# Optimization experiments

Hardware: AMD Instinct MI355X
Metric: run time of the kernel (lower is better)

## Reference

```python
import jax, jax.numpy as jnp
import numpy as np

N_HEAD = 16
N_EMBD = 1024
B, T = 4, 2048


def setup_inputs() -> dict:
    key = jax.random.key(0)
    ks = jax.random.split(key, 5)
    s_in = 1.0 / np.sqrt(N_EMBD)
    return {
        "x": jax.random.normal(ks[0], (B, T, N_EMBD), dtype=jnp.float32),
        "W_qkv": jax.random.normal(ks[1], (N_EMBD, 3 * N_EMBD), dtype=jnp.float32) * s_in,
        "b_qkv": jnp.zeros((3 * N_EMBD,), dtype=jnp.float32),
        "W_proj": jax.random.normal(ks[2], (N_EMBD, N_EMBD), dtype=jnp.float32) * s_in,
        "b_proj": jnp.zeros((N_EMBD,), dtype=jnp.float32),
    }


def reference(x, W_qkv, b_qkv, W_proj, b_proj):
    Bb, Tt, C = x.shape
    H = N_HEAD
    hd = C // H  # head dim
    qkv = x @ W_qkv + b_qkv                      # [B,T,3C]
    q, k, v = jnp.split(qkv, 3, axis=-1)
    # [B,H,T,hd]
    q = q.reshape(Bb, Tt, H, hd).transpose(0, 2, 1, 3)
    k = k.reshape(Bb, Tt, H, hd).transpose(0, 2, 1, 3)
    v = v.reshape(Bb, Tt, H, hd).transpose(0, 2, 1, 3)
    scale = 1.0 / np.sqrt(hd).astype(np.float32)
    att = jnp.einsum("bhqd,bhkd->bhqk", q, k) * scale
    causal = jnp.tril(jnp.ones((Tt, Tt), dtype=bool))
    att = jnp.where(causal, att, jnp.float32(-jnp.inf))
    att = jax.nn.softmax(att, axis=-1)
    y = jnp.einsum("bhqk,bhkd->bhqd", att, v)    # [B,H,T,hd]
    y = y.transpose(0, 2, 1, 3).reshape(Bb, Tt, C)
    return y @ W_proj + b_proj
```

## Files before the change

### kernel.cpp

```cpp
#include <hip/hip_runtime.h>
#include <hip/hip_bf16.h>
#include <math.h>

typedef unsigned short u16;
typedef __bf16 bf16_t;
typedef bf16_t bf16x8 __attribute__((ext_vector_type(8)));
typedef float f32x4 __attribute__((ext_vector_type(4)));

#define N_HEADC 16
#define C_EMBD  1024
#define B_SZ    4
#define T_SEQ   2048
#define HD      64
#define M_TOT   (B_SZ * T_SEQ)

__device__ __forceinline__ float b2f(u16 x) {
    return __uint_as_float(((unsigned)x) << 16);
}
__device__ __forceinline__ u16 f2b(float f) {
    unsigned u = __float_as_uint(f);
    u = u + 0x7fffu + ((u >> 16) & 1u);
    return (u16)(u >> 16);
}
__device__ __forceinline__ unsigned pack2f(float a, float b) {
    unsigned ua = (__float_as_uint(a) + 0x8000u) >> 16;
    unsigned ub = (__float_as_uint(b) + 0x8000u) & 0xffff0000u;
    return ua | ub;
}
__device__ __forceinline__ float fexp2(float x) {
#if __has_builtin(__builtin_amdgcn_exp2f)
    return __builtin_amdgcn_exp2f(x);
#else
    return exp2f(x);
#endif
}
__device__ __forceinline__ void gl_lds16(const u16* g, u16* l) {
    __builtin_amdgcn_global_load_lds(
        (const __attribute__((address_space(1))) unsigned int*)g,
        (__attribute__((address_space(3))) unsigned int*)l,
        16, 0, 0);
}


__global__ __launch_bounds__(256) void cast_f32_to_bf16(const float* __restrict__ in,
                                                        u16* __restrict__ out) {
    int i = (blockIdx.x * 256 + threadIdx.x) * 4;
    float4 v = *(const float4*)(in + i);
    ushort4 o;
    o.x = f2b(v.x); o.y = f2b(v.y); o.z = f2b(v.z); o.w = f2b(v.w);
    *(ushort4*)(out + i) = o;
}

__global__ __launch_bounds__(256) void transpose_cast(const float* __restrict__ in,
                                                      u16* __restrict__ out,
                                                      int K, int N) {
    __shared__ float tile[32][33];
    int n0 = blockIdx.x * 32, k0 = blockIdx.y * 32;
    for (int i = threadIdx.y; i < 32; i += 8)
        tile[i][threadIdx.x] = in[(size_t)(k0 + i) * N + n0 + threadIdx.x];
    __syncthreads();
    for (int i = threadIdx.y; i < 32; i += 8)
        out[(size_t)(n0 + i) * K + k0 + threadIdx.x] = f2b(tile[threadIdx.x][i]);
}

__global__ __launch_bounds__(256) void gemm_qkv(const u16* __restrict__ A,
                                                const u16* __restrict__ BT,
                                                const float* __restrict__ bias,
                                                u16* __restrict__ qQ,
                                                u16* __restrict__ qK,
                                                u16* __restrict__ qVt) {
    const int K = C_EMBD;
    __shared__ __align__(16) u16 sA[128 * 32];
    __shared__ __align__(16) u16 sB[128 * 32];
    int m0 = blockIdx.y * 128;
    int n0 = blockIdx.x * 128;
    int tid = threadIdx.x;
    int w = tid >> 6, lane = tid & 63;
    int m_off = (w & 1) * 64, n_off = (w >> 1) * 64;
    int quad = lane >> 4, rl = lane & 15;

    f32x4 acc[4][4];
    #pragma unroll
    for (int i = 0; i < 4; ++i)
        #pragma unroll
        for (int j = 0; j < 4; ++j)
            acc[i][j] = f32x4{0.f, 0.f, 0.f, 0.f};

    int srow = lane >> 2, sko = (lane & 3) * 8;

    for (int k0 = 0; k0 < K; k0 += 32) {
        #pragma unroll
        for (int c = 0; c < 4; ++c) {
            int rb = ((w & 1) * 4 + c) * 16;
            if (w < 2)
                gl_lds16(&A[(size_t)(m0 + rb + srow) * K + k0 + sko], &sA[rb * 32]);
            else
                gl_lds16(&BT[(size_t)(n0 + rb + srow) * K + k0 + sko], &sB[rb * 32]);
        }
        __syncthreads();
        bf16x8 af[4], bfr[4];
        #pragma unroll
        for (int i = 0; i < 4; ++i)
            af[i] = *(const bf16x8*)&sA[(m_off + i * 16 + rl) * 32 + quad * 8];
        #pragma unroll
        for (int j = 0; j < 4; ++j)
            bfr[j] = *(const bf16x8*)&sB[(n_off + j * 16 + rl) * 32 + quad * 8];
        #pragma unroll
        for (int i = 0; i < 4; ++i)
            #pragma unroll
            for (int j = 0; j < 4; ++j)
                acc[i][j] = __builtin_amdgcn_mfma_f32_16x16x32_bf16(af[i], bfr[j], acc[i][j], 0, 0, 0);
        __syncthreads();
    }

    const float QSC = 0.18033688011112042f;
    #pragma unroll
    for (int j = 0; j < 4; ++j) {
        int n = n0 + n_off + j * 16 + rl;
        float bv = bias[n];
        int p = n >> 10, cch = n & 1023;
        int h = cch >> 6, d = cch & 63;
        #pragma unroll
        for (int i = 0; i < 4; ++i) {
            int mbase = m0 + m_off + i * 16 + quad * 4;
            int bb = mbase >> 11, t0 = mbase & 2047;
            size_t thbase = ((size_t)bb * N_HEADC + h) * T_SEQ;
            if (p == 0) {
                #pragma unroll
                for (int r = 0; r < 4; ++r)
                    qQ[(thbase + t0 + r) * HD + d] = f2b((acc[i][j][r] + bv) * QSC);
            } else if (p == 1) {
                #pragma unroll
                for (int r = 0; r < 4; ++r)
                    qK[(thbase + t0 + r) * HD + d] = f2b(acc[i][j][r] + bv);
            } else {
                ushort4 o;
                o.x = f2b(acc[i][j][0] + bv);
                o.y = f2b(acc[i][j][1] + bv);
                o.z = f2b(acc[i][j][2] + bv);
                o.w = f2b(acc[i][j][3] + bv);
                *(ushort4*)&qVt[(((size_t)bb * N_HEADC + h) * HD + d) * T_SEQ + t0] = o;
            }
        }
    }
}

__global__ __launch_bounds__(256) void gemm_proj(const u16* __restrict__ A,
                                                 const u16* __restrict__ BT,
                                                 const float* __restrict__ bias,
                                                 float* __restrict__ out) {
    const int K = C_EMBD;
    __shared__ __align__(16) u16 sA[128 * 32];
    __shared__ __align__(16) u16 sB[128 * 32];
    int m0 = blockIdx.y * 128;
    int n0 = blockIdx.x * 128;
    int tid = threadIdx.x;
    int w = tid >> 6, lane = tid & 63;
    int m_off = (w & 1) * 64, n_off = (w >> 1) * 64;
    int quad = lane >> 4, rl = lane & 15;

    f32x4 acc[4][4];
    #pragma unroll
    for (int i = 0; i < 4; ++i)
        #pragma unroll
        for (int j = 0; j < 4; ++j)
            acc[i][j] = f32x4{0.f, 0.f, 0.f, 0.f};

    int srow = lane >> 2, sko = (lane & 3) * 8;

    for (int k0 = 0; k0 < K; k0 += 32) {
        #pragma unroll
        for (int c = 0; c < 4; ++c) {
            int rb = ((w & 1) * 4 + c) * 16;
            if (w < 2)
                gl_lds16(&A[(size_t)(m0 + rb + srow) * K + k0 + sko], &sA[rb * 32]);
            else
                gl_lds16(&BT[(size_t)(n0 + rb + srow) * K + k0 + sko], &sB[rb * 32]);
        }
        __syncthreads();
        bf16x8 af[4], bfr[4];
        #pragma unroll
        for (int i = 0; i < 4; ++i)
            af[i] = *(const bf16x8*)&sA[(m_off + i * 16 + rl) * 32 + quad * 8];
        #pragma unroll
        for (int j = 0; j < 4; ++j)
            bfr[j] = *(const bf16x8*)&sB[(n_off + j * 16 + rl) * 32 + quad * 8];
        #pragma unroll
        for (int i = 0; i < 4; ++i)
            #pragma unroll
            for (int j = 0; j < 4; ++j)
                acc[i][j] = __builtin_amdgcn_mfma_f32_16x16x32_bf16(af[i], bfr[j], acc[i][j], 0, 0, 0);
        __syncthreads();
    }

    #pragma unroll
    for (int i = 0; i < 4; ++i) {
        int mbase = m0 + m_off + i * 16 + quad * 4;
        #pragma unroll
        for (int j = 0; j < 4; ++j) {
            int n = n0 + n_off + j * 16 + rl;
            float bv = bias[n];
            #pragma unroll
            for (int r = 0; r < 4; ++r)
                out[(size_t)(mbase + r) * C_EMBD + n] = acc[i][j][r] + bv;
        }
    }
}

__global__ __launch_bounds__(256) void attn_mfma(const u16* __restrict__ Qg,
                                                 const u16* __restrict__ Kg,
                                                 const u16* __restrict__ Vtg,
                                                 u16* __restrict__ yb) {
    int bx = blockIdx.x, h = blockIdx.y, b = blockIdx.z;
    const size_t hs = (size_t)T_SEQ * HD;
    const u16* Qp  = Qg  + ((size_t)b * N_HEADC + h) * hs;
    const u16* Kp  = Kg  + ((size_t)b * N_HEADC + h) * hs;
    const u16* Vtp = Vtg + ((size_t)b * N_HEADC + h) * hs;

    __shared__ __align__(16) u16 sK[2][2][64][32];
    __shared__ __align__(16) u16 sVt[2][2][64][32];
    __shared__ __align__(16) u16 sP[4][32][72];

    int tid = threadIdx.x;
    int lane = tid & 63, w = tid >> 6;
    int quad = lane >> 4, rl = lane & 15;
    u16* sPw = &sP[w][0][0];
    int srow = lane >> 2;
    int sch = (lane & 3) * 8;
    const f32x4 zf = {0.f, 0.f, 0.f, 0.f};
    const float SOFT_M = 16.0f;

    #pragma unroll
    for (int phase = 0; phase < 2; ++phase) {
        int qt = phase == 0 ? (15 - bx) : bx;
        int q0w = qt * 128 + w * 32;
        int nkt = 2 * qt + 2;

        bf16x8 qf[2][2];
        #pragma unroll
        for (int nt = 0; nt < 2; ++nt)
            #pragma unroll
            for (int ks = 0; ks < 2; ++ks)
                qf[nt][ks] = *(const bf16x8*)&Qp[(size_t)(q0w + nt * 16 + rl) * HD + ks * 32 + quad * 8];

        f32x4 O[2][4];
        #pragma unroll
        for (int mi = 0; mi < 2; ++mi)
            #pragma unroll
            for (int nd = 0; nd < 4; ++nd)
                O[mi][nd] = f32x4{0.f, 0.f, 0.f, 0.f};
        float l_[2] = {0.f, 0.f};

        __syncthreads();
        #pragma unroll
        for (int c = 0; c < 4; ++c) {
            int lc = w * 4 + c;
            int ks = (lc >> 2) & 1;
            int rb = (lc & 3) * 16;
            if (lc < 8)
                gl_lds16(Kp + (size_t)(rb + srow) * HD + ks * 32 + sch, &sK[0][ks][rb][0]);
            else
                gl_lds16(Vtp + (size_t)(rb + srow) * T_SEQ + ks * 32 + sch, &sVt[0][ks][rb][0]);
        }

        for (int kt = 0; kt < nkt; ++kt) {
            __syncthreads();
            int buf = kt & 1;
            int k0 = kt * 64;
            if (kt + 1 < nkt) {
                int k1 = k0 + 64;
                #pragma unroll
                for (int c = 0; c < 4; ++c) {
                    int lc = w * 4 + c;
                    int ks = (lc >> 2) & 1;
                    int rb = (lc & 3) * 16;
                    if (lc < 8)
                        gl_lds16(Kp + (size_t)(k1 + rb + srow) * HD + ks * 32 + sch,
                                 &sK[buf ^ 1][ks][rb][0]);
                    else
                        gl_lds16(Vtp + (size_t)(rb + srow) * T_SEQ + k1 + ks * 32 + sch,
                                 &sVt[buf ^ 1][ks][rb][0]);
                }
            }
            if (k0 > q0w + 31) continue;

            f32x4 st[4][2];
            #pragma unroll
            for (int mt = 0; mt < 4; ++mt) {
                bf16x8 ak0 = *(const bf16x8*)&sK[buf][0][mt * 16 + rl][quad * 8];
                bf16x8 ak1 = *(const bf16x8*)&sK[buf][1][mt * 16 + rl][quad * 8];
                #pragma unroll
                for (int nt = 0; nt < 2; ++nt) {
                    f32x4 t = __builtin_amdgcn_mfma_f32_16x16x32_bf16(ak0, qf[nt][0], zf, 0, 0, 0);
                    st[mt][nt] = __builtin_amdgcn_mfma_f32_16x16x32_bf16(ak1, qf[nt][1], t, 0, 0, 0);
                }
            }

            if (k0 + 63 > q0w) {
                #pragma unroll
                for (int mt = 0; mt < 4; ++mt)
                    #pragma unroll
                    for (int nt = 0; nt < 2; ++nt)
                        #pragma unroll
                        for (int r = 0; r < 4; ++r) {
                            int kpos = k0 + mt * 16 + quad * 4 + r;
                            int q = q0w + nt * 16 + rl;
                            if (kpos > q) st[mt][nt][r] = -INFINITY;
                        }
            }

            #pragma unroll
            for (int nt = 0; nt < 2; ++nt) {
                float lsum = 0.f;
                #pragma unroll
                for (int mt = 0; mt < 4; ++mt) {
                    float p0 = fexp2(st[mt][nt][0] - SOFT_M);
                    float p1 = fexp2(st[mt][nt][1] - SOFT_M);
                    float p2 = fexp2(st[mt][nt][2] - SOFT_M);
                    float p3 = fexp2(st[mt][nt][3] - SOFT_M);
                    lsum += (p0 + p1) + (p2 + p3);
                    *(uint2*)&sPw[(nt * 16 + rl) * 72 + mt * 16 + quad * 4] =
                        make_uint2(pack2f(p0, p1), pack2f(p2, p3));
                }
                l_[nt] += lsum;
            }

            #pragma unroll
            for (int ks = 0; ks < 2; ++ks) {
                bf16x8 ap0 = *(const bf16x8*)&sPw[(0 * 16 + rl) * 72 + ks * 32 + quad * 8];
                bf16x8 ap1 = *(const bf16x8*)&sPw[(1 * 16 + rl) * 72 + ks * 32 + quad * 8];
                #pragma unroll
                for (int nd = 0; nd < 4; ++nd) {
                    bf16x8 bv = *(const bf16x8*)&sVt[buf][ks][nd * 16 + rl][quad * 8];
                    O[0][nd] = __builtin_amdgcn_mfma_f32_16x16x32_bf16(ap0, bv, O[0][nd], 0, 0, 0);
                    O[1][nd] = __builtin_amdgcn_mfma_f32_16x16x32_bf16(ap1, bv, O[1][nd], 0, 0, 0);
                }
            }
        }

        #pragma unroll
        for (int nt = 0; nt < 2; ++nt) {
            l_[nt] += __shfl_xor(l_[nt], 16);
            l_[nt] += __shfl_xor(l_[nt], 32);
        }
        float linv[2] = {1.f / l_[0], 1.f / l_[1]};
        int idxq = quad * 4;
        #pragma unroll
        for (int mi = 0; mi < 2; ++mi)
            #pragma unroll
            for (int r = 0; r < 4; ++r) {
                float li = __shfl(linv[mi], idxq + r);
                int qg = q0w + mi * 16 + quad * 4 + r;
                size_t base = ((size_t)b * T_SEQ + qg) * C_EMBD + h * HD;
                #pragma unroll
                for (int nd = 0; nd < 4; ++nd)
                    yb[base + nd * 16 + rl] = f2b(O[mi][nd][r] * li);
            }
    }
}

extern "C" void kernel_launch(void* const* d_in, const int* in_sizes, int n_in,
                              void* d_out, int out_size, void* d_ws, size_t ws_size,
                              hipStream_t stream) {
    const float* x     = (const float*)d_in[0];
    const float* Wqkv  = (const float*)d_in[1];
    const float* bqkv  = (const float*)d_in[2];
    const float* Wproj = (const float*)d_in[3];
    const float* bproj = (const float*)d_in[4];
    float* out = (float*)d_out;

    char* ws = (char*)d_ws;
    u16* xb     = (u16*)(ws);
    u16* WqkvT  = (u16*)(ws + (size_t)16 * 1024 * 1024);
    u16* WprojT = (u16*)(ws + (size_t)22 * 1024 * 1024);
    u16* qQ     = (u16*)(ws + (size_t)24 * 1024 * 1024);
    u16* qK     = (u16*)(ws + (size_t)40 * 1024 * 1024);
    u16* qVt    = (u16*)(ws + (size_t)56 * 1024 * 1024);
    u16* yb     = (u16*)(ws + (size_t)72 * 1024 * 1024);

    cast_f32_to_bf16<<<dim3(M_TOT * C_EMBD / (256 * 4)), dim3(256), 0, stream>>>(x, xb);
    transpose_cast<<<dim3(3 * C_EMBD / 32, C_EMBD / 32), dim3(32, 8), 0, stream>>>(
        Wqkv, WqkvT, C_EMBD, 3 * C_EMBD);
    transpose_cast<<<dim3(C_EMBD / 32, C_EMBD / 32), dim3(32, 8), 0, stream>>>(
        Wproj, WprojT, C_EMBD, C_EMBD);
    gemm_qkv<<<dim3(3 * C_EMBD / 128, M_TOT / 128), dim3(256), 0, stream>>>(
        xb, WqkvT, bqkv, qQ, qK, qVt);
    attn_mfma<<<dim3(8, N_HEADC, B_SZ), dim3(256), 0, stream>>>(
        qQ, qK, qVt, yb);
    gemm_proj<<<dim3(C_EMBD / 128, M_TOT / 128), dim3(256), 0, stream>>>(
        yb, WprojT, bproj, out);
}
```

Baseline: 271.0 us.

## Split attention into one q-tile per block, add separate V transpose kernel

The attention kernel no longer pairs two q-tiles per block. It launches 16 blocks per head, with the heaviest tiles scheduled first, which raises parallelism and removes the phase loop. The QKV GEMM now writes V in row layout with uniform stores, and a new transpose kernel builds V^T in place of the scattered transposed stores. The change also folds the softmax offset into the MFMA accumulator init, uses the hardware packed bf16 convert, and pads the P tile. It adds an extra kernel launch and a pass over V, and the qV buffer reuses the yb region.

Measured after the change: 340.7 us. 1.26x slower.

```diff
diff --git a/kernel.cpp b/kernel.cpp
--- a/kernel.cpp
+++ b/kernel.cpp
@@ -14,18 +14,15 @@
 #define HD      64
 #define M_TOT   (B_SZ * T_SEQ)
 
-__device__ __forceinline__ float b2f(u16 x) {
-    return __uint_as_float(((unsigned)x) << 16);
-}
 __device__ __forceinline__ u16 f2b(float f) {
     unsigned u = __float_as_uint(f);
     u = u + 0x7fffu + ((u >> 16) & 1u);
     return (u16)(u >> 16);
 }
-__device__ __forceinline__ unsigned pack2f(float a, float b) {
-    unsigned ua = (__float_as_uint(a) + 0x8000u) >> 16;
-    unsigned ub = (__float_as_uint(b) + 0x8000u) & 0xffff0000u;
-    return ua | ub;
+__device__ __forceinline__ unsigned pkbf16(float a, float b) {
+    unsigned d;
+    asm("v_cvt_pk_bf16_f32 %0, %1, %2" : "=v"(d) : "v"(a), "v"(b));
+    return d;
 }
 __device__ __forceinline__ float fexp2(float x) {
 #if __has_builtin(__builtin_amdgcn_exp2f)
@@ -63,12 +60,37 @@
         out[(size_t)(n0 + i) * K + k0 + threadIdx.x] = f2b(tile[threadIdx.x][i]);
 }
 
+__global__ __launch_bounds__(256) void transpose_v(const u16* __restrict__ qV,
+                                                   u16* __restrict__ qVt) {
+    __shared__ u16 tile[64][66];
+    int t0 = blockIdx.x * 64;
+    size_t base = (size_t)blockIdx.y * T_SEQ * HD;
+    int tid = threadIdx.x;
+    #pragma unroll
+    for (int c = 0; c < 2; ++c) {
+        int ch = tid * 2 + c;
+        int row = ch >> 3, off = (ch & 7) * 8;
+        uint4 v = *(const uint4*)&qV[base + (size_t)(t0 + row) * HD + off];
+        const unsigned* pv = (const unsigned*)&v;
+        #pragma unroll
+        for (int e = 0; e < 4; ++e)
+            *(unsigned*)&tile[row][off + e * 2] = pv[e];
+    }
+    __syncthreads();
+    int d = tid >> 2, tq = tid & 3;
+    u16 vals[16];
+    #pragma unroll
+    for (int k = 0; k < 16; ++k) vals[k] = tile[tq * 16 + k][d];
+    *(uint4*)&qVt[base + (size_t)d * T_SEQ + t0 + tq * 16] = *(uint4*)&vals[0];
+    *(uint4*)&qVt[base + (size_t)d * T_SEQ + t0 + tq * 16 + 8] = *(uint4*)&vals[8];
+}
+
 __global__ __launch_bounds__(256) void gemm_qkv(const u16* __restrict__ A,
                                                 const u16* __restrict__ BT,
                                                 const float* __restrict__ bias,
                                                 u16* __restrict__ qQ,
                                                 u16* __restrict__ qK,
-                                                u16* __restrict__ qVt) {
+                                                u16* __restrict__ qV) {
     const int K = C_EMBD;
     __shared__ __align__(16) u16 sA[128 * 32];
     __shared__ __align__(16) u16 sB[128 * 32];
@@ -120,27 +142,16 @@
         float bv = bias[n];
         int p = n >> 10, cch = n & 1023;
         int h = cch >> 6, d = cch & 63;
+        u16* dst = p == 0 ? qQ : (p == 1 ? qK : qV);
+        float sc = p == 0 ? QSC : 1.0f;
         #pragma unroll
         for (int i = 0; i < 4; ++i) {
             int mbase = m0 + m_off + i * 16 + quad * 4;
             int bb = mbase >> 11, t0 = mbase & 2047;
             size_t thbase = ((size_t)bb * N_HEADC + h) * T_SEQ;
-            if (p == 0) {
-                #pragma unroll
-                for (int r = 0; r < 4; ++r)
-                    qQ[(thbase + t0 + r) * HD + d] = f2b((acc[i][j][r] + bv) * QSC);
-            } else if (p == 1) {
-                #pragma unroll
-                for (int r = 0; r < 4; ++r)
-                    qK[(thbase + t0 + r) * HD + d] = f2b(acc[i][j][r] + bv);
-            } else {
-                ushort4 o;
-                o.x = f2b(acc[i][j][0] + bv);
-                o.y = f2b(acc[i][j][1] + bv);
-                o.z = f2b(acc[i][j][2] + bv);
-                o.w = f2b(acc[i][j][3] + bv);
-                *(ushort4*)&qVt[(((size_t)bb * N_HEADC + h) * HD + d) * T_SEQ + t0] = o;
-            }
+            #pragma unroll
+            for (int r = 0; r < 4; ++r)
+                dst[(thbase + t0 + r) * HD + d] = f2b((acc[i][j][r] + bv) * sc);
         }
     }
 }
@@ -211,7 +222,7 @@
                                                  const u16* __restrict__ Kg,
                                                  const u16* __restrict__ Vtg,
                                                  u16* __restrict__ yb) {
-    int bx = blockIdx.x, h = blockIdx.y, b = blockIdx.z;
+    int qt = 15 - blockIdx.x, h = blockIdx.y, b = blockIdx.z;
     const size_t hs = (size_t)T_SEQ * HD;
     const u16* Qp  = Qg  + ((size_t)b * N_HEADC + h) * hs;
     const u16* Kp  = Kg  + ((size_t)b * N_HEADC + h) * hs;
@@ -219,7 +230,7 @@
 
     __shared__ __align__(16) u16 sK[2][2][64][32];
     __shared__ __align__(16) u16 sVt[2][2][64][32];
-    __shared__ __align__(16) u16 sP[4][32][72];
+    __shared__ __align__(16) u16 sP[4][32][76];
 
     int tid = threadIdx.x;
     int lane = tid & 63, w = tid >> 6;
@@ -227,136 +238,129 @@
     u16* sPw = &sP[w][0][0];
     int srow = lane >> 2;
     int sch = (lane & 3) * 8;
-    const f32x4 zf = {0.f, 0.f, 0.f, 0.f};
-    const float SOFT_M = 16.0f;
-
-    #pragma unroll
-    for (int phase = 0; phase < 2; ++phase) {
-        int qt = phase == 0 ? (15 - bx) : bx;
-        int q0w = qt * 128 + w * 32;
-        int nkt = 2 * qt + 2;
-
-        bf16x8 qf[2][2];
-        #pragma unroll
-        for (int nt = 0; nt < 2; ++nt)
-            #pragma unroll
-            for (int ks = 0; ks < 2; ++ks)
-                qf[nt][ks] = *(const bf16x8*)&Qp[(size_t)(q0w + nt * 16 + rl) * HD + ks * 32 + quad * 8];
-
-        f32x4 O[2][4];
-        #pragma unroll
-        for (int mi = 0; mi < 2; ++mi)
+    const f32x4 mneg = {-16.f, -16.f, -16.f, -16.f};
+    int q0w = qt * 128 + w * 32;
+    int nkt = 2 * qt + 2;
+
+    bf16x8 qf[2][2];
+    #pragma unroll
+    for (int nt = 0; nt < 2; ++nt)
+        #pragma unroll
+        for (int ks = 0; ks < 2; ++ks)
+            qf[nt][ks] = *(const bf16x8*)&Qp[(size_t)(q0w + nt * 16 + rl) * HD + ks * 32 + quad * 8];
+
+    f32x4 O[2][4];
+    #pragma unroll
+    for (int mi = 0; mi < 2; ++mi)
+        #pragma unroll
+        for (int nd = 0; nd < 4; ++nd)
+            O[mi][nd] = f32x4{0.f, 0.f, 0.f, 0.f};
+    float l_[2] = {0.f, 0.f};
+
+    #pragma unroll
+    for (int c = 0; c < 4; ++c) {
+        int lc = w * 4 + c;
+        int ks = (lc >> 2) & 1;
+        int rb = (lc & 3) * 16;
+        if (lc < 8)
+            gl_lds16(Kp + (size_t)(rb + srow) * HD + ks * 32 + sch, &sK[0][ks][rb][0]);
+        else
+            gl_lds16(Vtp + (size_t)(rb + srow) * T_SEQ + ks * 32 + sch, &sVt[0][ks][rb][0]);
+    }
+
+    for (int kt = 0; kt < nkt; ++kt) {
+        __syncthreads();
+        int buf = kt & 1;
+        int k0 = kt * 64;
+        if (kt + 1 < nkt) {
+            int k1 = k0 + 64;
+            #pragma unroll
+            for (int c = 0; c < 4; ++c) {
+                int lc = w * 4 + c;
+                int ks = (lc >> 2) & 1;
+                int rb = (lc & 3) * 16;
+                if (lc < 8)
+                    gl_lds16(Kp + (size_t)(k1 + rb + srow) * HD + ks * 32 + sch,
+                             &sK[buf ^ 1][ks][rb][0]);
+                else
+                    gl_lds16(Vtp + (size_t)(rb + srow) * T_SEQ + k1 + ks * 32 + sch,
+                             &sVt[buf ^ 1][ks][rb][0]);
+            }
+        }
+        if (k0 > q0w + 31) continue;
+
+        f32x4 st[4][2];
+        #pragma unroll
+        for (int mt = 0; mt < 4; ++mt) {
+            bf16x8 ak0 = *(const bf16x8*)&sK[buf][0][mt * 16 + rl][quad * 8];
+            bf16x8 ak1 = *(const bf16x8*)&sK[buf][1][mt * 16 + rl][quad * 8];
+            #pragma unroll
+            for (int nt = 0; nt < 2; ++nt) {
+                f32x4 t = __builtin_amdgcn_mfma_f32_16x16x32_bf16(ak0, qf[nt][0], mneg, 0, 0, 0);
+                st[mt][nt] = __builtin_amdgcn_mfma_f32_16x16x32_bf16(ak1, qf[nt][1], t, 0, 0, 0);
+            }
+        }
+
+        if (k0 + 63 > q0w) {
+            #pragma unroll
+            for (int mt = 0; mt < 4; ++mt)
+                #pragma unroll
+                for (int nt = 0; nt < 2; ++nt)
+                    #pragma unroll
+                    for (int r = 0; r < 4; ++r) {
+                        int kpos = k0 + mt * 16 + quad * 4 + r;
+                        int q = q0w + nt * 16 + rl;
+                        if (kpos > q) st[mt][nt][r] = -INFINITY;
+                    }
+        }
+
+        #pragma unroll
+        for (int nt = 0; nt < 2; ++nt) {
+            float lsum = 0.f;
+            #pragma unroll
+            for (int mt = 0; mt < 4; ++mt) {
+                float p0 = fexp2(st[mt][nt][0]);
+                float p1 = fexp2(st[mt][nt][1]);
+                float p2 = fexp2(st[mt][nt][2]);
+                float p3 = fexp2(st[mt][nt][3]);
+                lsum += (p0 + p1) + (p2 + p3);
+                *(uint2*)&sPw[(nt * 16 + rl) * 76 + mt * 16 + quad * 4] =
+                    make_uint2(pkbf16(p0, p1), pkbf16(p2, p3));
+            }
+            l_[nt] += lsum;
+        }
+
+        #pragma unroll
+        for (int ks = 0; ks < 2; ++ks) {
+            bf16x8 ap0 = *(const bf16x8*)&sPw[(0 * 16 + rl) * 76 + ks * 32 + quad * 8];
+            bf16x8 ap1 = *(const bf16x8*)&sPw[(1 * 16 + rl) * 76 + ks * 32 + quad * 8];
+            #pragma unroll
+            for (int nd = 0; nd < 4; ++nd) {
+                bf16x8 bv = *(const bf16x8*)&sVt[buf][ks][nd * 16 + rl][quad * 8];
+                O[0][nd] = __builtin_amdgcn_mfma_f32_16x16x32_bf16(ap0, bv, O[0][nd], 0, 0, 0);
+                O[1][nd] = __builtin_amdgcn_mfma_f32_16x16x32_bf16(ap1, bv, O[1][nd], 0, 0, 0);
+            }
+        }
+    }
+
+    #pragma unroll
+    for (int nt = 0; nt < 2; ++nt) {
+        l_[nt] += __shfl_xor(l_[nt], 16);
+        l_[nt] += __shfl_xor(l_[nt], 32);
+    }
+    float linv[2] = {1.f / l_[0], 1.f / l_[1]};
+    int idxq = quad * 4;
+    #pragma unroll
+    for (int mi = 0; mi < 2; ++mi)
+        #pragma unroll
+        for (int r = 0; r < 4; ++r) {
+            float li = __shfl(linv[mi], idxq + r);
+            int qg = q0w + mi * 16 + quad * 4 + r;
+            size_t base = ((size_t)b * T_SEQ + qg) * C_EMBD + h * HD;
             #pragma unroll
             for (int nd = 0; nd < 4; ++nd)
-                O[mi][nd] = f32x4{0.f, 0.f, 0.f, 0.f};
-        float l_[2] = {0.f, 0.f};
-
-        __syncthreads();
-        #pragma unroll
-        for (int c = 0; c < 4; ++c) {
-            int lc = w * 4 + c;
-            int ks = (lc >> 2) & 1;
-            int rb = (lc & 3) * 16;
-            if (lc < 8)
-                gl_lds16(Kp + (size_t)(rb + srow) * HD + ks * 32 + sch, &sK[0][ks][rb][0]);
-            else
-                gl_lds16(Vtp + (size_t)(rb + srow) * T_SEQ + ks * 32 + sch, &sVt[0][ks][rb][0]);
-        }
-
-        for (int kt = 0; kt < nkt; ++kt) {
-            __syncthreads();
-            int buf = kt & 1;
-            int k0 = kt * 64;
-            if (kt + 1 < nkt) {
-                int k1 = k0 + 64;
-                #pragma unroll
-                for (int c = 0; c < 4; ++c) {
-                    int lc = w * 4 + c;
-                    int ks = (lc >> 2) & 1;
-                    int rb = (lc & 3) * 16;
-                    if (lc < 8)
-                        gl_lds16(Kp + (size_t)(k1 + rb + srow) * HD + ks * 32 + sch,
-                                 &sK[buf ^ 1][ks][rb][0]);
-                    else
-                        gl_lds16(Vtp + (size_t)(rb + srow) * T_SEQ + k1 + ks * 32 + sch,
-                                 &sVt[buf ^ 1][ks][rb][0]);
-                }
-            }
-            if (k0 > q0w + 31) continue;
-
-            f32x4 st[4][2];
-            #pragma unroll
-            for (int mt = 0; mt < 4; ++mt) {
-                bf16x8 ak0 = *(const bf16x8*)&sK[buf][0][mt * 16 + rl][quad * 8];
-                bf16x8 ak1 = *(const bf16x8*)&sK[buf][1][mt * 16 + rl][quad * 8];
-                #pragma unroll
-                for (int nt = 0; nt < 2; ++nt) {
-                    f32x4 t = __builtin_amdgcn_mfma_f32_16x16x32_bf16(ak0, qf[nt][0], zf, 0, 0, 0);
-                    st[mt][nt] = __builtin_amdgcn_mfma_f32_16x16x32_bf16(ak1, qf[nt][1], t, 0, 0, 0);
-                }
-            }
-
-            if (k0 + 63 > q0w) {
-                #pragma unroll
-                for (int mt = 0; mt < 4; ++mt)
-                    #pragma unroll
-                    for (int nt = 0; nt < 2; ++nt)
-                        #pragma unroll
-                        for (int r = 0; r < 4; ++r) {
-                            int kpos = k0 + mt * 16 + quad * 4 + r;
-                            int q = q0w + nt * 16 + rl;
-                            if (kpos > q) st[mt][nt][r] = -INFINITY;
-                        }
-            }
-
-            #pragma unroll
-            for (int nt = 0; nt < 2; ++nt) {
-                float lsum = 0.f;
-                #pragma unroll
-                for (int mt = 0; mt < 4; ++mt) {
-                    float p0 = fexp2(st[mt][nt][0] - SOFT_M);
-                    float p1 = fexp2(st[mt][nt][1] - SOFT_M);
-                    float p2 = fexp2(st[mt][nt][2] - SOFT_M);
-                    float p3 = fexp2(st[mt][nt][3] - SOFT_M);
-                    lsum += (p0 + p1) + (p2 + p3);
-                    *(uint2*)&sPw[(nt * 16 + rl) * 72 + mt * 16 + quad * 4] =
-                        make_uint2(pack2f(p0, p1), pack2f(p2, p3));
-                }
-                l_[nt] += lsum;
-            }
-
-            #pragma unroll
-            for (int ks = 0; ks < 2; ++ks) {
-                bf16x8 ap0 = *(const bf16x8*)&sPw[(0 * 16 + rl) * 72 + ks * 32 + quad * 8];
-                bf16x8 ap1 = *(const bf16x8*)&sPw[(1 * 16 + rl) * 72 + ks * 32 + quad * 8];
-                #pragma unroll
-                for (int nd = 0; nd < 4; ++nd) {
-                    bf16x8 bv = *(const bf16x8*)&sVt[buf][ks][nd * 16 + rl][quad * 8];
-                    O[0][nd] = __builtin_amdgcn_mfma_f32_16x16x32_bf16(ap0, bv, O[0][nd], 0, 0, 0);
-                    O[1][nd] = __builtin_amdgcn_mfma_f32_16x16x32_bf16(ap1, bv, O[1][nd], 0, 0, 0);
-                }
-            }
-        }
-
-        #pragma unroll
-        for (int nt = 0; nt < 2; ++nt) {
-            l_[nt] += __shfl_xor(l_[nt], 16);
-            l_[nt] += __shfl_xor(l_[nt], 32);
-        }
-        float linv[2] = {1.f / l_[0], 1.f / l_[1]};
-        int idxq = quad * 4;
-        #pragma unroll
-        for (int mi = 0; mi < 2; ++mi)
-            #pragma unroll
-            for (int r = 0; r < 4; ++r) {
-                float li = __shfl(linv[mi], idxq + r);
-                int qg = q0w + mi * 16 + quad * 4 + r;
-                size_t base = ((size_t)b * T_SEQ + qg) * C_EMBD + h * HD;
-                #pragma unroll
-                for (int nd = 0; nd < 4; ++nd)
-                    yb[base + nd * 16 + rl] = f2b(O[mi][nd][r] * li);
-            }
-    }
+                yb[base + nd * 16 + rl] = f2b(O[mi][nd][r] * li);
+        }
 }
 
 extern "C" void kernel_launch(void* const* d_in, const int* in_sizes, int n_in,
@@ -377,6 +381,7 @@
     u16* qK     = (u16*)(ws + (size_t)40 * 1024 * 1024);
     u16* qVt    = (u16*)(ws + (size_t)56 * 1024 * 1024);
     u16* yb     = (u16*)(ws + (size_t)72 * 1024 * 1024);
+    u16* qV     = yb;
 
     cast_f32_to_bf16<<<dim3(M_TOT * C_EMBD / (256 * 4)), dim3(256), 0, stream>>>(x, xb);
     transpose_cast<<<dim3(3 * C_EMBD / 32, C_EMBD / 32), dim3(32, 8), 0, stream>>>(
@@ -384,8 +389,9 @@
     transpose_cast<<<dim3(C_EMBD / 32, C_EMBD / 32), dim3(32, 8), 0, stream>>>(
         Wproj, WprojT, C_EMBD, C_EMBD);
     gemm_qkv<<<dim3(3 * C_EMBD / 128, M_TOT / 128), dim3(256), 0, stream>>>(
-        xb, WqkvT, bqkv, qQ, qK, qVt);
-    attn_mfma<<<dim3(8, N_HEADC, B_SZ), dim3(256), 0, stream>>>(
+        xb, WqkvT, bqkv, qQ, qK, qV);
+    transpose_v<<<dim3(T_SEQ / 64, B_SZ * N_HEADC), dim3(256), 0, stream>>>(qV, qVt);
+    attn_mfma<<<dim3(16, N_HEADC, B_SZ), dim3(256), 0, stream>>>(
         qQ, qK, qVt, yb);
     gemm_proj<<<dim3(C_EMBD / 128, M_TOT / 128), dim3(256), 0, stream>>>(
         yb, WprojT, bproj, out);
```
